# Performance work log

Hardware: AMD Instinct MI355X
Metric: run time of the kernel (lower is better)

The kernel has to match this reference:

```python
import jax, jax.numpy as jnp
import numpy as np

B, N, DIM, H, DH = 2, 1024, 2048, 16, 128
MAX_POS = 16
QK_SCALE = 10.0  # qk_norm_scale (replaces dim_head**-0.5 when qk_norm=True)
NEG = -1e30  # large negative mask value (sigmoid -> 0, softmax -> 0)

def rotate_half(x):
    # interleaved pair rotation: '... (d r) -> ... d r', r=2
    shape = x.shape
    xr = x.reshape(shape[:-1] + (shape[-1] // 2, 2))
    x1, x2 = xr[..., 0], xr[..., 1]
    return jnp.stack((-x2, x1), axis=-1).reshape(shape)

def setup_inputs() -> dict:
    key = jax.random.key(0)
    ks = jax.random.split(key, 10)
    # proper rotary frequencies, repeat-interleaved to match rotate_half's pair layout
    half = DH // 2
    inv_freq = 1.0 / (10000.0 ** (np.arange(half, dtype=np.float32) / half))
    freqs = np.repeat(np.outer(np.arange(N, dtype=np.float32), inv_freq), 2, axis=-1)  # [N, DH]
    sd = 0.02
    return {
        'x': jax.random.normal(ks[0], (B, N, DIM), jnp.float32),
        'rotary_freqs': jnp.asarray(freqs),
        'w_q': jax.random.normal(ks[1], (DIM, H * DH), jnp.float32) * sd,
        'w_k': jax.random.normal(ks[2], (DIM, H * DH), jnp.float32) * sd,
        'w_v': jax.random.normal(ks[3], (DIM, H * DH), jnp.float32) * sd,
        'cope_emb': jax.random.normal(ks[4], (MAX_POS, DH), jnp.float32) * sd,  # CoPE pos_emb (nonzero for testing)
        'th_pre': jnp.eye(H, dtype=jnp.float32) + jax.random.normal(ks[5], (H, H), jnp.float32) * sd,
        'th_post': jnp.eye(H, dtype=jnp.float32) + jax.random.normal(ks[6], (H, H), jnp.float32) * sd,
        'w_vgate': jax.random.normal(ks[7], (DIM, H * DH), jnp.float32) * sd,
        'b_vgate': jnp.full((H * DH,), 10.0, jnp.float32),
        'w_hgate': jax.random.normal(ks[8], (DIM, H), jnp.float32) * sd,
        'b_hgate': jnp.full((H,), 10.0, jnp.float32),
        'w_out': jax.random.normal(ks[9], (H * DH, DIM), jnp.float32) * sd,
    }

def reference(x, rotary_freqs, w_q, w_k, w_v, cope_emb, th_pre, th_post, w_vgate, b_vgate, w_hgate, b_hgate, w_out):
    b, n, _ = x.shape
    to_heads = lambda t: t.reshape(b, n, H, DH).transpose(0, 2, 1, 3)  # b h n d
    q = to_heads(x @ w_q)
    k = to_heads(x @ w_k)
    v = to_heads(x @ w_v)
    # qk l2-norm (groups=1), then fixed qk_norm_scale
    q = q / jnp.maximum(jnp.linalg.norm(q, axis=-1, keepdims=True), 1e-12)
    k = k / jnp.maximum(jnp.linalg.norm(k, axis=-1, keepdims=True), 1e-12)
    # rotary embedding (scale=1, rot_dim == dim_head)
    cos, sin = jnp.cos(rotary_freqs), jnp.sin(rotary_freqs)
    q = q * cos + rotate_half(q) * sin
    k = k * cos + rotate_half(k) * sin
    sim = jnp.einsum('bhid,bhjd->bhij', q, k) * QK_SCALE
    sim = jnp.einsum('hg,bgij->bhij', th_pre, sim)  # pre-softmax talking heads (1x1 conv over heads)
    causal = jnp.triu(jnp.ones((n, n), dtype=bool), 1)
    sim = jnp.where(causal, NEG, sim)
    # ---- CoPE (linear interpolation path) ----
    gates = jax.nn.sigmoid(sim)  # masked entries -> 0
    pos = jnp.flip(jnp.cumsum(jnp.flip(gates, -1), axis=-1), -1)  # reverse cumsum over j
    pos = jnp.minimum(pos, MAX_POS - 1.0)
    logits_int = jnp.einsum('bhnd,pd->bhnp', q, cope_emb)
    pos_floor = jnp.floor(pos)
    w_interp = pos - pos_floor
    lc = jnp.take_along_axis(logits_int, jnp.ceil(pos).astype(jnp.int32), axis=-1)
    lf = jnp.take_along_axis(logits_int, pos_floor.astype(jnp.int32), axis=-1)
    sim = sim + lc * w_interp + lf * (1.0 - w_interp)
    # ------------------------------------------
    attn = jax.nn.softmax(sim, axis=-1)
    attn = jnp.einsum('hg,bgij->bhij', th_post, attn)  # post-softmax talking heads
    out = jnp.einsum('bhij,bhjd->bhid', attn, v)
    # per-head value gate
    head_gate = jax.nn.sigmoid(x @ w_hgate + b_hgate)  # b n h
    out = out * head_gate.transpose(0, 2, 1)[..., None]
    out = out.transpose(0, 2, 1, 3).reshape(b, n, H * DH)
    # elementwise value gate (sigmoid, bias init 10)
    out = out * jax.nn.sigmoid(x @ w_vgate + b_vgate)
    return out @ w_out
```

## Files before the change

### kernel.cpp

```cpp
#include <hip/hip_runtime.h>
#include <hip/hip_fp16.h>

typedef unsigned short u16;
typedef __attribute__((ext_vector_type(4))) float f32x4;
typedef __attribute__((ext_vector_type(8))) _Float16 f16x8;
typedef __attribute__((ext_vector_type(4))) _Float16 f16x4;
typedef __attribute__((ext_vector_type(8))) unsigned short u16x8;
typedef __attribute__((ext_vector_type(4))) unsigned short u16x4;

#define DEVI __device__ __forceinline__
#define MASKV (-1000.0f)

DEVI u16 f2h(float f){ __half h = __float2half(f); return __half_as_ushort(h); }
DEVI float h2f(u16 v){ return __half2float(__ushort_as_half(v)); }
DEVI float sigm(float s){ float e = __expf(-fabsf(s)); return (s >= 0.f) ? 1.f/(1.f+e) : e/(1.f+e); }

DEVI void async16(const void* g, void* l){
  __builtin_amdgcn_global_load_lds((__attribute__((address_space(1))) const unsigned int*)g,
                                   (__attribute__((address_space(3))) unsigned int*)l, 16, 0, 0);
}

struct PrepArgs {
  const float* src[7];
  u16* dst[7];
  int C[7];
};
__global__ __launch_bounds__(256) void k_prep(PrepArgs p){
  __shared__ u16 t[64][65];
  int z = blockIdx.z;
  int tid = threadIdx.x;
  if (z == 0){
    size_t b0 = (size_t)(blockIdx.y*32 + blockIdx.x)*4096;
    #pragma unroll
    for (int c = 0; c < 4; c++){
      size_t ix = b0 + (size_t)(c*256 + tid)*4;
      f32x4 v = *(const f32x4*)(p.src[0] + ix);
      u16x4 o;
      #pragma unroll
      for (int e=0; e<4; e++) o[e] = f2h(v[e]);
      *(u16x4*)(p.dst[0] + ix) = o;
    }
    return;
  }
  const float* src = p.src[z]; u16* dst = p.dst[z];
  int C = p.C[z];
  int c0 = blockIdx.x*64, r0 = blockIdx.y*64;
  if (c0 >= C) return;
  int tx = tid & 15, ty = tid >> 4;
  #pragma unroll
  for (int rr = 0; rr < 4; rr++){
    int r = r0 + rr*16 + ty, c = c0 + tx*4;
    if (c < C){
      f32x4 v = *(const f32x4*)(src + (size_t)r*C + c);
      #pragma unroll
      for (int e=0; e<4; e++) t[rr*16+ty][tx*4+e] = f2h(v[e]);
    }
  }
  __syncthreads();
  #pragma unroll
  for (int rr = 0; rr < 4; rr++){
    int rr2 = c0 + rr*16 + ty;
    if (rr2 < C){
      u16x4 o;
      #pragma unroll
      for (int e=0; e<4; e++) o[e] = t[tx*4+e][rr*16+ty];
      *(u16x4*)(dst + (size_t)rr2*2048 + r0 + tx*4) = o;
    }
  }
}

struct ProjArgs {
  const u16* xh;
  const u16* wT0; const u16* wT1; const u16* wT2; const u16* wT3;
  u16* q; u16* k; u16* v; u16* vg;
  const float* bvg;
};
__global__ __launch_bounds__(512) void k_proj2(ProjArgs p){
  __shared__ __align__(16) u16 ldsA[2][16384];
  __shared__ __align__(16) u16 ldsB[2][16384];
  const int z = blockIdx.z;
  const u16* wT = (z==0) ? p.wT0 : (z==1) ? p.wT1 : (z==2) ? p.wT2 : p.wT3;
  const int m0 = blockIdx.x << 8, n0 = blockIdx.y << 8;
  const int tid = threadIdx.x, w = tid >> 6, l = tid & 63;
  const int wm = w >> 2, wn = w & 3, qq = l >> 4, m = l & 15;
  const int cxor = (m & 7) * 8;
  const int lrow = l >> 3;
  const int lcol = (((l & 7) ^ (l >> 3)) * 8);
  const u16* aSrc = p.xh + (size_t)(m0 + lrow) * 2048 + lcol;
  const u16* bSrc = wT   + (size_t)(n0 + lrow) * 2048 + lcol;
  const int wp2 = w * 2;

  f32x4 acc[8][4];
  { f32x4 zr = {0.f,0.f,0.f,0.f};
    #pragma unroll
    for (int i=0;i<8;i++)
      #pragma unroll
      for (int j=0;j<4;j++) acc[i][j] = zr; }

#define STGA(buf,h,kt) do{ \
    async16(aSrc + (size_t)((h)*128 + wp2*8)*2048 + (kt)*64,     &ldsA[buf][(h)*8192 + wp2*512]); \
    async16(aSrc + (size_t)((h)*128 + (wp2+1)*8)*2048 + (kt)*64, &ldsA[buf][(h)*8192 + (wp2+1)*512]); }while(0)
#define STGB(buf,h,kt) do{ \
    async16(bSrc + (size_t)((h)*128 + wp2*8)*2048 + (kt)*64,     &ldsB[buf][(h)*8192 + wp2*512]); \
    async16(bSrc + (size_t)((h)*128 + (wp2+1)*8)*2048 + (kt)*64, &ldsB[buf][(h)*8192 + (wp2+1)*512]); }while(0)
#define RDA(buf,i,s) (*(const f16x8*)(&ldsA[buf][(wm*128 + (i)*16 + m)*64 + (((s)*32 + qq*8) ^ cxor)]))
#define RDB(buf,j,s) (*(const f16x8*)(&ldsB[buf][(wn*64 + (j)*16 + m)*64 + (((s)*32 + qq*8) ^ cxor)]))

  f16x8 bf[4][2];
#define RDBALL(buf) do{ \
    _Pragma("unroll") \
    for (int j=0;j<4;j++){ bf[j][0] = RDB(buf,j,0); bf[j][1] = RDB(buf,j,1); } }while(0)
#define VMW asm volatile("s_waitcnt vmcnt(4)" ::: "memory")
#define PHASE(buf,i0,BSTMT,SSTMT,VMSTMT) do{ \
    f16x8 a00 = RDA(buf,(i0),0),   a01 = RDA(buf,(i0),1); \
    f16x8 a10 = RDA(buf,(i0)+1,0), a11 = RDA(buf,(i0)+1,1); \
    BSTMT; \
    SSTMT; \
    __builtin_amdgcn_s_barrier(); \
    asm volatile("s_waitcnt lgkmcnt(0)" ::: "memory"); \
    __builtin_amdgcn_s_setprio(1); \
    _Pragma("unroll") \
    for (int j=0;j<4;j++){ \
      acc[(i0)][j]   = __builtin_amdgcn_mfma_f32_16x16x32_f16(a00, bf[j][0], acc[(i0)][j],   0,0,0); \
      acc[(i0)+1][j] = __builtin_amdgcn_mfma_f32_16x16x32_f16(a10, bf[j][0], acc[(i0)+1][j], 0,0,0); \
    } \
    _Pragma("unroll") \
    for (int j=0;j<4;j++){ \
      acc[(i0)][j]   = __builtin_amdgcn_mfma_f32_16x16x32_f16(a01, bf[j][1], acc[(i0)][j],   0,0,0); \
      acc[(i0)+1][j] = __builtin_amdgcn_mfma_f32_16x16x32_f16(a11, bf[j][1], acc[(i0)+1][j], 0,0,0); \
    } \
    __builtin_amdgcn_s_setprio(0); \
    VMSTMT; \
    __builtin_amdgcn_s_barrier(); }while(0)

  STGA(0,0,0); STGA(0,1,0); STGB(0,0,0); STGB(0,1,0); STGB(1,0,1); STGB(1,1,1);
  VMW;
  __builtin_amdgcn_s_barrier();

  for (int u = 0; u < 16; u++){
    const int t1 = 2*u+1, t2 = (2*u+2)&31, t3 = (2*u+3)&31;
    PHASE(0,0, RDBALL(0), STGA(1,0,t1), ((void)0));
    PHASE(0,2, ((void)0), STGA(1,1,t1), ((void)0));
    PHASE(0,4, ((void)0), STGB(0,0,t2), ((void)0));
    PHASE(0,6, ((void)0), STGB(0,1,t2), VMW);
    PHASE(1,0, RDBALL(1), STGA(0,0,t2), ((void)0));
    PHASE(1,2, ((void)0), STGA(0,1,t2), ((void)0));
    PHASE(1,4, ((void)0), STGB(1,0,t3), ((void)0));
    PHASE(1,6, ((void)0), STGB(1,1,t3), VMW);
  }

  u16* dst3 = (z==0) ? p.q : (z==1) ? p.k : p.v;
  #pragma unroll
  for (int i=0;i<8;i++)
  #pragma unroll
  for (int j=0;j<4;j++)
  #pragma unroll
  for (int r=0;r<4;r++){
    int gr = m0 + wm*128 + i*16 + qq*4 + r;
    int gc = n0 + wn*64 + j*16 + m;
    float v = acc[i][j][r];
    if (z == 3){
      p.vg[(size_t)gr*2048 + gc] = f2h(sigm(v + p.bvg[gc]));
    } else {
      int b = gr >> 10, ii = gr & 1023, h = gc >> 7, d = gc & 127;
      dst3[(((size_t)(b*16 + h))*1024 + ii)*128 + d] = f2h(v);
    }
  }
#undef STGA
#undef STGB
#undef RDA
#undef RDB
#undef RDBALL
#undef VMW
#undef PHASE
}

struct MidArgs {
  const u16* xh; const u16* whgT; const float* bhg; float* hg;
  const u16* vb; u16* vTT;
  u16* qb; u16* kb; const float* freqs; const float* cope; float* L;
};
__global__ __launch_bounds__(256) void k_mid(MidArgs p){
  __shared__ float red[4][256];
  __shared__ u16 t[32][33];
  __shared__ float ce[2048];
  int bz = blockIdx.x;
  int tid = threadIdx.x;
  if (bz < 128){
    int w = tid>>6, l = tid&63, q = l>>4, m = l&15;
    int t0 = bz*16;
    f32x4 acc = {0.f,0.f,0.f,0.f};
    const u16* xr = p.xh   + (size_t)(t0 + m)*2048 + w*512;
    const u16* br = p.whgT + (size_t)m*2048 + w*512;
    #pragma unroll 4
    for (int k = 0; k < 512; k += 32){
      f16x8 a = *(const f16x8*)(xr + k + q*8);
      f16x8 b = *(const f16x8*)(br + k + q*8);
      acc = __builtin_amdgcn_mfma_f32_16x16x32_f16(a, b, acc, 0, 0, 0);
    }
    #pragma unroll
    for (int r = 0; r < 4; r++) red[w][(q*4+r)*16 + m] = acc[r];
    __syncthreads();
    float v = red[0][tid] + red[1][tid] + red[2][tid] + red[3][tid];
    int tl = tid >> 4, h = tid & 15;
    p.hg[(size_t)(t0 + tl)*16 + h] = sigm(v + p.bhg[h]);
    return;
  }
  if (bz < 4224){
    int f = bz - 128;
    int zb = f >> 7, rem = f & 127;
    int by = rem >> 2, bx = rem & 3;
    const u16* src = p.vb + (size_t)zb*131072;
    u16* dst = p.vTT + (size_t)zb*131072;
    int c0 = bx*32, r0 = by*32;
    int tx = tid & 31, ty = tid >> 5;
    #pragma unroll
    for (int i = ty; i < 32; i += 8){
      int r = r0 + i, c = c0 + tx;
      t[i][tx] = src[(size_t)r*128 + c];
    }
    __syncthreads();
    #pragma unroll
    for (int i = ty; i < 32; i += 8){
      int rr = c0 + i, cc = r0 + tx;
      dst[(size_t)rr*1024 + cc] = t[tx][i];
    }
    return;
  }
  {
    int bx = bz - 4224;
    if (bx < 8192){
      for (int i2 = tid; i2 < 2048; i2 += 256) ce[i2] = p.cope[i2];
    }
    __syncthreads();
    int w = tid >> 6, l = tid & 63;
    int r = bx*4 + w;
    int isq = (r < 32768) ? 1 : 0;
    int rr = isq ? r : r - 32768;
    int i = rr & 1023;
    u16* base = (isq ? p.qb : p.kb) + (size_t)rr*128;
    float v0 = h2f(base[2*l]), v1 = h2f(base[2*l+1]);
    float ss = v0*v0 + v1*v1;
    #pragma unroll
    for (int off = 1; off < 64; off <<= 1) ss += __shfl_xor(ss, off);
    float rn = 1.f / fmaxf(sqrtf(ss), 1e-12f);
    v0 *= rn; v1 *= rn;
    float f = p.freqs[i*128 + 2*l];
    float sn, cs; sincosf(f, &sn, &cs);
    float o0 = v0*cs - v1*sn, o1 = v1*cs + v0*sn;
    base[2*l] = f2h(o0); base[2*l+1] = f2h(o1);
    if (isq){
      #pragma unroll
      for (int pp = 0; pp < 16; pp++){
        float part = o0*ce[pp*128 + 2*l] + o1*ce[pp*128 + 2*l + 1];
        #pragma unroll
        for (int off = 1; off < 64; off <<= 1) part += __shfl_xor(part, off);
        if (l == pp) p.L[(size_t)rr*16 + pp] = part;
      }
    }
  }
}

__global__ __launch_bounds__(256) void k_qk(const u16* __restrict__ qb, const u16* __restrict__ kb,
    u16* __restrict__ S){
  __shared__ __align__(16) u16 As[8192];
  __shared__ __align__(16) u16 Bs[16384];
  int bh = blockIdx.y;
  int bx = 15 - (int)blockIdx.x;
  int i0 = bx*64, it = bx >> 1;
  int njt = (bx + 2) >> 1;
  int tid = threadIdx.x, w = tid>>6, l = tid&63, q = l>>4, m = l&15, wm = w&1, wn = w>>1;
  const u16* qbase = qb + (size_t)bh*131072;
  const u16* kbase = kb + (size_t)bh*131072;
  #pragma unroll
  for (int sub = 0; sub < 4; sub++){
    int row = w*16 + (l>>2);
    async16(qbase + (size_t)(i0 + row)*128 + sub*32 + (l&3)*8, As + sub*2048 + (w*16)*32);
  }
  u16* dstbase = S + ((size_t)bh*36 + (it*(it+1))/2)*16384 + (size_t)((bx&1)*64)*128;
  for (int jt = 0; jt < njt; jt++){
    __syncthreads();
    #pragma unroll
    for (int sub = 0; sub < 4; sub++)
      #pragma unroll
      for (int p = 0; p < 2; p++){
        int row = w*32 + p*16 + (l>>2);
        async16(kbase + (size_t)(jt*128 + row)*128 + sub*32 + (l&3)*8,
                Bs + sub*4096 + (w*32 + p*16)*32);
      }
    __syncthreads();
    f32x4 acc[2][4];
    { f32x4 z = {0.f,0.f,0.f,0.f};
      #pragma unroll
      for (int a2=0;a2<2;a2++)
        #pragma unroll
        for (int b2=0;b2<4;b2++) acc[a2][b2] = z; }
    #pragma unroll
    for (int kc = 0; kc < 4; kc++){
      f16x8 af[2], bf[4];
      #pragma unroll
      for (int t = 0; t < 2; t++) af[t] = *(const f16x8*)(As + kc*2048 + (wm*32 + t*16 + m)*32 + q*8);
      #pragma unroll
      for (int t = 0; t < 4; t++) bf[t] = *(const f16x8*)(Bs + kc*4096 + (wn*64 + t*16 + m)*32 + q*8);
      #pragma unroll
      for (int a2 = 0; a2 < 2; a2++)
        #pragma unroll
        for (int b2 = 0; b2 < 4; b2++)
          acc[a2][b2] = __builtin_amdgcn_mfma_f32_16x16x32_f16(af[a2], bf[b2], acc[a2][b2], 0, 0, 0);
    }
    u16* dst = dstbase + (size_t)jt*16384;
    #pragma unroll
    for (int ti=0; ti<2; ti++)
    #pragma unroll
    for (int tj=0; tj<4; tj++)
    #pragma unroll
    for (int r=0; r<4; r++){
      int iloc = wm*32 + ti*16 + q*4 + r;
      int jloc = wn*64 + tj*16 + m;
      float v = acc[ti][tj][r] * 10.f;
      if (jt*128 + jloc > i0 + iloc) v = MASKV;
      dst[(size_t)iloc*128 + jloc] = f2h(v);
    }
  }
}

struct CopeArgs { const u16* S; const float* L; const float* thpre; u16* Sout; float* ml; };
__global__ __launch_bounds__(1024) void k_cope(CopeArgs pa){
  __shared__ u16 raw[16*276];
  __shared__ float thsh[256];
  __shared__ float Lsh[1024];
  int b = blockIdx.y;
  int i0 = (int)(gridDim.x - 1 - blockIdx.x) * 4;
  int tid = threadIdx.x, w = tid>>6, l = tid&63;
  int h = w;
  if (tid < 256) thsh[tid] = pa.thpre[tid];
  Lsh[tid] = pa.L[ ((size_t)((b*16 + (tid>>6))*1024) + i0 + ((tid>>4)&3))*16 + (tid&15) ];
  __syncthreads();
  float th_r[16];
  #pragma unroll
  for (int g = 0; g < 16; g++) th_r[g] = thsh[h*16 + g];
  int ii = l >> 4, j0 = (l & 15)*4;
  int i = i0 + ii, it1 = i >> 7, iloc = i & 127;
  const float* Lrow = Lsh + h*64 + ii*16;
  float carry = 0.f, mrun = -1e30f, lrun = 0.f;
  int tmax = (i0 + 3) >> 6;
  for (int t = tmax; t >= 0; t--){
    int jt1 = (t*64) >> 7, jo = (t*64) & 127;
    __syncthreads();
    {
      int e = tid*4;
      int g = e >> 8, r = e & 255;
      int si = r >> 6, j = r & 63;
      int irow = i0 + si; int it2 = irow >> 7, il2 = irow & 127;
      const u16* src = pa.S + ((size_t)((b*16+g)*36 + (it2*(it2+1))/2 + jt1))*16384
                           + (size_t)il2*128 + jo + j;
      *(u16x4*)(raw + g*276 + si*68 + j) = *(const u16x4*)src;
    }
    __syncthreads();
    float s0=0.f, s1=0.f, s2=0.f, s3=0.f;
    #pragma unroll
    for (int g = 0; g < 16; g++){
      u16x4 v = *(const u16x4*)(raw + g*276 + ii*68 + j0);
      float tg = th_r[g];
      s0 += tg*h2f(v[0]); s1 += tg*h2f(v[1]); s2 += tg*h2f(v[2]); s3 += tg*h2f(v[3]);
    }
    float g0 = sigm(s0), g1 = sigm(s1), g2 = sigm(s2), g3 = sigm(s3);
    float c3 = g3, c2 = g2 + c3, c1 = g1 + c2, c0 = g0 + c1;
    float T = c0, Tacc = T;
    #pragma unroll
    for (int off = 1; off < 16; off <<= 1){
      float tv = __shfl(Tacc, (l + off) & 63);
      if (((l & 15) + off) < 16) Tacc += tv;
    }
    float Rh = Tacc - T;
    float rowtot = __shfl(Tacc, l & 48);
    float sf[4];
    float cc[4] = {c0, c1, c2, c3};
    float ssv[4] = {s0, s1, s2, s3};
    #pragma unroll
    for (int c = 0; c < 4; c++){
      float pos = fminf(cc[c] + Rh + carry, 15.f);
      float pf = floorf(pos);
      float wi = pos - pf;
      int ic = (int)ceilf(pos), ifl = (int)pf;
      float v = ssv[c] + Lrow[ic]*wi + Lrow[ifl]*(1.f - wi);
      sf[c] = v;
    }
    carry += rowtot;
    u16x4 ov;
    #pragma unroll
    for (int c = 0; c < 4; c++){ ov[c] = f2h(sf[c]); sf[c] = h2f(ov[c]); }
    *(u16x4*)(pa.Sout + ((size_t)((b*16+h)*36 + (it1*(it1+1))/2 + jt1))*16384
              + (size_t)iloc*128 + jo + j0) = ov;
    float M = fmaxf(fmaxf(sf[0], sf[1]), fmaxf(sf[2], sf[3]));
    #pragma unroll
    for (int off = 1; off < 16; off <<= 1) M = fmaxf(M, __shfl_xor(M, off));
    float mnew = fmaxf(mrun, M);
    float es = __expf(fminf(sf[0]-mnew,0.f)) + __expf(fminf(sf[1]-mnew,0.f))
             + __expf(fminf(sf[2]-mnew,0.f)) + __expf(fminf(sf[3]-mnew,0.f));
    #pragma unroll
    for (int off = 1; off < 16; off <<= 1) es += __shfl_xor(es, off);
    lrun = lrun*__expf(fminf(mrun - mnew, 0.f)) + es;
    mrun = mnew;
  }
  if ((l & 15) == 0){
    size_t bix = (size_t)(b*16 + h)*1024 + i0 + ii;
    pa.ml[bix] = mrun;
    pa.ml[32768 + bix] = 1.f/fmaxf(lrun, 1e-30f);
  }
}

struct PostArgs { const u16* S; const float* ml; const float* thpost; u16* Sout; };
__global__ __launch_bounds__(256) void k_postmix(PostArgs pa){
  __shared__ u16 at[16*1040];
  __shared__ _Float16 thsh[256];
  __shared__ float mh[128], rlh[128];
  int tile = blockIdx.x >> 4, sub = blockIdx.x & 15, b = blockIdx.y;
  int it = 0;
  #pragma unroll
  for (int t2=1; t2<8; t2++) if (tile >= (t2*(t2+1))/2) it = t2;
  int tid = threadIdx.x;
  thsh[tid] = (_Float16)pa.thpost[tid];
  if (tid < 128){
    int g = tid >> 3, ii = tid & 7;
    size_t ix = (size_t)(b*16+g)*1024 + it*128 + sub*8 + ii;
    mh[tid] = pa.ml[ix]; rlh[tid] = pa.ml[32768 + ix];
  }
  __syncthreads();
  {
    int g = tid >> 4, l16 = tid & 15;
    const u16* src = pa.S + ((size_t)((b*16+g)*36 + tile))*16384 + sub*1024;
    #pragma unroll
    for (int c = 0; c < 16; c++){
      int e = c*64 + l16*4;
      int ii = e >> 7;
      float mm = mh[g*8+ii], rr = rlh[g*8+ii];
      u16x4 sv = *(const u16x4*)(src + e);
      u16x4 o;
      #pragma unroll
      for (int z2=0; z2<4; z2++) o[z2] = f2h(__expf(fminf(h2f(sv[z2]) - mm, 0.f)) * rr);
      *(u16x4*)(at + g*1040 + e) = o;
    }
  }
  __syncthreads();
  int h = tid >> 4, c16 = tid & 15;
  _Float16 th_h[16];
  #pragma unroll
  for (int g = 0; g < 16; g++) th_h[g] = thsh[h*16 + g];
  u16* dst = pa.Sout + ((size_t)((b*16+h)*36 + tile))*16384 + sub*1024;
  #pragma unroll
  for (int k = 0; k < 16; k++){
    int e = c16*4 + k*64;
    f16x4 a = {0,0,0,0};
    #pragma unroll
    for (int g = 0; g < 16; g++){
      f16x4 v = *(const f16x4*)(at + g*1040 + e);
      a += v * th_h[g];
    }
    *(f16x4*)(dst + e) = a;
  }
}

struct PvArgs { const u16* S; const u16* vT; const float* hg; const u16* vg; u16* gated; };
__global__ __launch_bounds__(256) void k_pv(PvArgs pa){
  __shared__ __align__(16) u16 As[8192];
  __shared__ __align__(16) u16 Bs[16384];
  int bh = blockIdx.y, b = bh >> 4, h = bh & 15;
  int bx = 15 - (int)blockIdx.x;
  int i0 = bx*64, it = bx >> 1;
  int nc = (bx + 2) >> 1;
  int tid = threadIdx.x, w = tid>>6, l = tid&63, q = l>>4, m = l&15, wm = w&1, wn = w>>1;
  const u16* abase = pa.S + ((size_t)bh*36 + (it*(it+1))/2)*16384 + (size_t)((bx&1)*64)*128;
  const u16* vt    = pa.vT + (size_t)bh*131072;
  f32x4 acc[2][4];
  { f32x4 z = {0.f,0.f,0.f,0.f};
    #pragma unroll
    for (int a2=0;a2<2;a2++)
      #pragma unroll
      for (int b2=0;b2<4;b2++) acc[a2][b2] = z; }
  for (int jc = 0; jc < nc; jc++){
    __syncthreads();
    #pragma unroll
    for (int sub = 0; sub < 4; sub++){
      int row = w*16 + (l>>2);
      async16(abase + (size_t)jc*16384 + (size_t)row*128 + sub*32 + (l&3)*8,
              As + sub*2048 + (w*16)*32);
      #pragma unroll
      for (int p = 0; p < 2; p++){
        int brow = w*32 + p*16 + (l>>2);
        async16(vt + (size_t)brow*1024 + jc*128 + sub*32 + (l&3)*8,
                Bs + sub*4096 + (w*32 + p*16)*32);
      }
    }
    __syncthreads();
    #pragma unroll
    for (int kc = 0; kc < 4; kc++){
      f16x8 af[2], bf[4];
      #pragma unroll
      for (int t = 0; t < 2; t++) af[t] = *(const f16x8*)(As + kc*2048 + (wm*32 + t*16 + m)*32 + q*8);
      #pragma unroll
      for (int t = 0; t < 4; t++) bf[t] = *(const f16x8*)(Bs + kc*4096 + (wn*64 + t*16 + m)*32 + q*8);
      #pragma unroll
      for (int a2 = 0; a2 < 2; a2++)
        #pragma unroll
        for (int b2 = 0; b2 < 4; b2++)
          acc[a2][b2] = __builtin_amdgcn_mfma_f32_16x16x32_f16(af[a2], bf[b2], acc[a2][b2], 0, 0, 0);
    }
  }
  #pragma unroll
  for (int ti=0; ti<2; ti++)
  #pragma unroll
  for (int tj=0; tj<4; tj++)
  #pragma unroll
  for (int r=0; r<4; r++){
    int i = i0 + wm*32 + ti*16 + q*4 + r;
    int d = wn*64 + tj*16 + m;
    int tok = b*1024 + i;
    float v = acc[ti][tj][r] * pa.hg[(size_t)tok*16 + h] * h2f(pa.vg[(size_t)tok*2048 + h*128 + d]);
    if (v != v) v = 333.f;
    pa.gated[(size_t)tok*2048 + h*128 + d] = f2h(v);
  }
}

__global__ __launch_bounds__(256) void k_out(const u16* __restrict__ gated, const u16* __restrict__ woT,
    float* __restrict__ out){
  __shared__ __align__(16) u16 As[2048];
  __shared__ __align__(16) u16 Bs[4096];
  int bx = blockIdx.x;
  int by = blockIdx.y;
  int trow0 = by*64, c0 = bx*128;
  int kbase = blockIdx.z * 1024;
  int tid = threadIdx.x, w = tid>>6, l = tid&63, q = l>>4, m = l&15, wm = w&1, wn = w>>1;
  f32x4 acc[2][4];
  { f32x4 z = {0.f,0.f,0.f,0.f};
    #pragma unroll
    for (int a2=0;a2<2;a2++)
      #pragma unroll
      for (int b2=0;b2<4;b2++) acc[a2][b2] = z; }
  for (int k0 = kbase; k0 < kbase + 1024; k0 += 32){
    __syncthreads();
    {
      int row = w*16 + (l>>2);
      async16(gated + (size_t)(trow0 + row)*2048 + k0 + (l&3)*8, As + (w*16)*32);
    }
    #pragma unroll
    for (int p = 0; p < 2; p++){
      int row = w*32 + p*16 + (l>>2);
      async16(woT + (size_t)(c0 + row)*2048 + k0 + (l&3)*8, Bs + (w*32 + p*16)*32);
    }
    __syncthreads();
    f16x8 af[2], bf[4];
    #pragma unroll
    for (int t = 0; t < 2; t++) af[t] = *(const f16x8*)(As + (wm*32 + t*16 + m)*32 + q*8);
    #pragma unroll
    for (int t = 0; t < 4; t++) bf[t] = *(const f16x8*)(Bs + (wn*64 + t*16 + m)*32 + q*8);
    #pragma unroll
    for (int a2 = 0; a2 < 2; a2++)
      #pragma unroll
      for (int b2 = 0; b2 < 4; b2++)
        acc[a2][b2] = __builtin_amdgcn_mfma_f32_16x16x32_f16(af[a2], bf[b2], acc[a2][b2], 0, 0, 0);
  }
  #pragma unroll
  for (int ti=0; ti<2; ti++)
  #pragma unroll
  for (int tj=0; tj<4; tj++)
  #pragma unroll
  for (int r=0; r<4; r++){
    int trow = trow0 + wm*32 + ti*16 + q*4 + r;
    int col  = c0 + wn*64 + tj*16 + m;
    float o = acc[ti][tj][r];
    if (o != o) o = 911.f;
    atomicAdd(&out[(size_t)trow*2048 + col], o);
  }
}

extern "C" void kernel_launch(void* const* d_in, const int* in_sizes, int n_in,
                              void* d_out, int out_size, void* d_ws, size_t ws_size,
                              hipStream_t stream){
  const float* x      = (const float*)d_in[0];
  const float* freqs  = (const float*)d_in[1];
  const float* w_q    = (const float*)d_in[2];
  const float* w_k    = (const float*)d_in[3];
  const float* w_v    = (const float*)d_in[4];
  const float* cope   = (const float*)d_in[5];
  const float* thpre  = (const float*)d_in[6];
  const float* thpost = (const float*)d_in[7];
  const float* w_vg   = (const float*)d_in[8];
  const float* b_vg   = (const float*)d_in[9];
  const float* w_hg   = (const float*)d_in[10];
  const float* b_hg   = (const float*)d_in[11];
  const float* w_out  = (const float*)d_in[12];

  char* ws = (char*)d_ws;
  size_t off = 0;
  auto alloc = [&](size_t bytes)->char*{ char* r = ws + off; off += (bytes + 255) & ~(size_t)255; return r; };
  u16*   xh    = (u16*)  alloc(8388608);
  u16*   wqT   = (u16*)  alloc(8388608);
  u16*   wkT   = (u16*)  alloc(8388608);
  u16*   wvT   = (u16*)  alloc(8388608);
  u16*   wvgT  = (u16*)  alloc(8388608);
  u16*   woT   = (u16*)  alloc(8388608);
  u16*   whgT  = (u16*)  alloc(65536);
  u16*   qb    = (u16*)  alloc(8388608);
  u16*   kb    = (u16*)  alloc(8388608);
  u16*   vb    = (u16*)  alloc(8388608);
  u16*   vTT   = (u16*)  alloc(8388608);
  u16*   vg    = (u16*)  alloc(8388608);
  u16*   gated = (u16*)  alloc(8388608);
  float* L     = (float*)alloc(2097152);
  float* hg    = (float*)alloc(131072);
  float* ml    = (float*)alloc(262144);
  u16*   S     = (u16*)  alloc(37748736);

  dim3 b256(256);
  PrepArgs pp;
  pp.src[0]=x;    pp.dst[0]=xh;   pp.C[0]=2048;
  pp.src[1]=w_q;  pp.dst[1]=wqT;  pp.C[1]=2048;
  pp.src[2]=w_k;  pp.dst[2]=wkT;  pp.C[2]=2048;
  pp.src[3]=w_v;  pp.dst[3]=wvT;  pp.C[3]=2048;
  pp.src[4]=w_vg; pp.dst[4]=wvgT; pp.C[4]=2048;
  pp.src[5]=w_out;pp.dst[5]=woT;  pp.C[5]=2048;
  pp.src[6]=w_hg; pp.dst[6]=whgT; pp.C[6]=16;
  k_prep<<<dim3(32,32,7), b256, 0, stream>>>(pp);

  ProjArgs pa{ xh, wqT, wkT, wvT, wvgT, qb, kb, vb, vg, b_vg };
  k_proj2<<<dim3(8,8,4), dim3(512), 0, stream>>>(pa);
  MidArgs ma{ xh, whgT, b_hg, hg, vb, vTT, qb, kb, freqs, cope, L };
  k_mid<<<dim3(20608), b256, 0, stream>>>(ma);
  k_qk<<<dim3(16,32), b256, 0, stream>>>(qb, kb, S);
  CopeArgs ca{ S, L, thpre, S, ml };
  k_cope<<<dim3(256,2), dim3(1024), 0, stream>>>(ca);
  PostArgs po{ S, ml, thpost, S };
  k_postmix<<<dim3(576,2), b256, 0, stream>>>(po);
  PvArgs pv{ S, vTT, hg, vg, gated };
  k_pv<<<dim3(16,32), b256, 0, stream>>>(pv);
  hipMemsetAsync(d_out, 0, out_size, stream);
  k_out<<<dim3(16,32,2), b256, 0, stream>>>(gated, woT, (float*)d_out);
}
```

Baseline: 469.1 us.

## Fuse softmax normalization and post-softmax talking-heads mix into CoPE kernel

```diff
diff --git a/kernel.cpp b/kernel.cpp
--- a/kernel.cpp
+++ b/kernel.cpp
@@ -324,16 +324,17 @@
   }
 }
 
-struct CopeArgs { const u16* S; const float* L; const float* thpre; u16* Sout; float* ml; };
+struct CopeArgs { const u16* S; const float* L; const float* thpre; const float* thpost; u16* Sout; };
 __global__ __launch_bounds__(1024) void k_cope(CopeArgs pa){
   __shared__ u16 raw[16*276];
   __shared__ float thsh[256];
+  __shared__ _Float16 thps[256];
   __shared__ float Lsh[1024];
   int b = blockIdx.y;
   int i0 = (int)(gridDim.x - 1 - blockIdx.x) * 4;
   int tid = threadIdx.x, w = tid>>6, l = tid&63;
   int h = w;
-  if (tid < 256) thsh[tid] = pa.thpre[tid];
+  if (tid < 256){ thsh[tid] = pa.thpre[tid]; thps[tid] = (_Float16)pa.thpost[tid]; }
   Lsh[tid] = pa.L[ ((size_t)((b*16 + (tid>>6))*1024) + i0 + ((tid>>4)&3))*16 + (tid&15) ];
   __syncthreads();
   float th_r[16];
@@ -403,61 +404,30 @@
     lrun = lrun*__expf(fminf(mrun - mnew, 0.f)) + es;
     mrun = mnew;
   }
-  if ((l & 15) == 0){
-    size_t bix = (size_t)(b*16 + h)*1024 + i0 + ii;
-    pa.ml[bix] = mrun;
-    pa.ml[32768 + bix] = 1.f/fmaxf(lrun, 1e-30f);
-  }
-}
-
-struct PostArgs { const u16* S; const float* ml; const float* thpost; u16* Sout; };
-__global__ __launch_bounds__(256) void k_postmix(PostArgs pa){
-  __shared__ u16 at[16*1040];
-  __shared__ _Float16 thsh[256];
-  __shared__ float mh[128], rlh[128];
-  int tile = blockIdx.x >> 4, sub = blockIdx.x & 15, b = blockIdx.y;
-  int it = 0;
-  #pragma unroll
-  for (int t2=1; t2<8; t2++) if (tile >= (t2*(t2+1))/2) it = t2;
-  int tid = threadIdx.x;
-  thsh[tid] = (_Float16)pa.thpost[tid];
-  if (tid < 128){
-    int g = tid >> 3, ii = tid & 7;
-    size_t ix = (size_t)(b*16+g)*1024 + it*128 + sub*8 + ii;
-    mh[tid] = pa.ml[ix]; rlh[tid] = pa.ml[32768 + ix];
-  }
-  __syncthreads();
-  {
-    int g = tid >> 4, l16 = tid & 15;
-    const u16* src = pa.S + ((size_t)((b*16+g)*36 + tile))*16384 + sub*1024;
-    #pragma unroll
-    for (int c = 0; c < 16; c++){
-      int e = c*64 + l16*4;
-      int ii = e >> 7;
-      float mm = mh[g*8+ii], rr = rlh[g*8+ii];
-      u16x4 sv = *(const u16x4*)(src + e);
-      u16x4 o;
-      #pragma unroll
-      for (int z2=0; z2<4; z2++) o[z2] = f2h(__expf(fminf(h2f(sv[z2]) - mm, 0.f)) * rr);
-      *(u16x4*)(at + g*1040 + e) = o;
-    }
-  }
-  __syncthreads();
-  int h = tid >> 4, c16 = tid & 15;
-  _Float16 th_h[16];
-  #pragma unroll
-  for (int g = 0; g < 16; g++) th_h[g] = thsh[h*16 + g];
-  u16* dst = pa.Sout + ((size_t)((b*16+h)*36 + tile))*16384 + sub*1024;
-  #pragma unroll
-  for (int k = 0; k < 16; k++){
-    int e = c16*4 + k*64;
+  float rl = 1.f / fmaxf(lrun, 1e-30f);
+  _Float16 tp_h[16];
+  #pragma unroll
+  for (int g = 0; g < 16; g++) tp_h[g] = thps[h*16 + g];
+  int t2max = it1*2 + 1;
+  for (int t = 0; t <= t2max; t++){
+    int jt1 = (t*64) >> 7, jo = (t*64) & 127;
+    u16* addr = pa.Sout + ((size_t)((b*16+h)*36 + (it1*(it1+1))/2 + jt1))*16384
+                        + (size_t)iloc*128 + jo + j0;
+    u16x4 sv = *(const u16x4*)addr;
+    u16x4 pv4;
+    #pragma unroll
+    for (int c = 0; c < 4; c++)
+      pv4[c] = f2h(__expf(fminf(h2f(sv[c]) - mrun, 0.f)) * rl);
+    __syncthreads();
+    *(u16x4*)(raw + h*276 + ii*68 + j0) = pv4;
+    __syncthreads();
     f16x4 a = {0,0,0,0};
     #pragma unroll
     for (int g = 0; g < 16; g++){
-      f16x4 v = *(const f16x4*)(at + g*1040 + e);
-      a += v * th_h[g];
-    }
-    *(f16x4*)(dst + e) = a;
+      f16x4 v = *(const f16x4*)(raw + g*276 + ii*68 + j0);
+      a += v * tp_h[g];
+    }
+    *(f16x4*)addr = a;
   }
 }
 
@@ -609,7 +579,6 @@
   u16*   gated = (u16*)  alloc(8388608);
   float* L     = (float*)alloc(2097152);
   float* hg    = (float*)alloc(131072);
-  float* ml    = (float*)alloc(262144);
   u16*   S     = (u16*)  alloc(37748736);
 
   dim3 b256(256);
@@ -628,10 +597,8 @@
   MidArgs ma{ xh, whgT, b_hg, hg, vb, vTT, qb, kb, freqs, cope, L };
   k_mid<<<dim3(20608), b256, 0, stream>>>(ma);
   k_qk<<<dim3(16,32), b256, 0, stream>>>(qb, kb, S);
-  CopeArgs ca{ S, L, thpre, S, ml };
+  CopeArgs ca{ S, L, thpre, thpost, S };
   k_cope<<<dim3(256,2), dim3(1024), 0, stream>>>(ca);
-  PostArgs po{ S, ml, thpost, S };
-  k_postmix<<<dim3(576,2), b256, 0, stream>>>(po);
   PvArgs pv{ S, vTT, hg, vg, gated };
   k_pv<<<dim3(16,32), b256, 0, stream>>>(pv);
   hipMemsetAsync(d_out, 0, out_size, stream);
```

New measurement: 468.9 us. About the same (-0.0%).
